# Optimization experiments

Hardware: AMD Instinct MI355X
Metric: run time of the kernel (lower is better)

Reference implementation:

```python
import jax, jax.numpy as jnp
import numpy as np

N, E = 100000, 1600000
DIMS = [128, 64, 64, 64, 32]  # in, hid, hid, hid, out
NEG_SLOPE = 0.2               # GATv2Conv default negative_slope
ELU_ALPHA_OUT = float(DIMS[-1])  # nn.ELU(out_channels): alpha = out_channels


def setup_inputs() -> dict:
    key = jax.random.key(0)
    ks = jax.random.split(key, 16)
    inp = {
        "x": jax.random.normal(ks[0], (N, DIMS[0]), dtype=jnp.float32),
        "edge_index": jax.random.randint(ks[1], (2, E), 0, N, dtype=jnp.int64),
    }
    ki = 2
    for i in range(4):
        fin, fout = DIMS[i], DIMS[i + 1]
        s = 1.0 / np.sqrt(fin)
        inp[f"Wl{i+1}"] = jax.random.uniform(ks[ki], (fin, fout), jnp.float32, -s, s); ki += 1
        inp[f"Wr{i+1}"] = jax.random.uniform(ks[ki], (fin, fout), jnp.float32, -s, s); ki += 1
        inp[f"att{i+1}"] = jax.random.uniform(ks[ki], (fout,), jnp.float32, -s, s); ki += 1
    return inp


def gatv2_layer(x, src, dst, Wl, Wr, att):
    # single head, concat=False, no self-loops, no bias (per module config)
    xl = x @ Wl                                   # [N, F] source-side projection
    xr = x @ Wr                                   # [N, F] target-side projection
    e = jax.nn.leaky_relu(xl[src] + xr[dst], NEG_SLOPE)   # [E, F]
    score = e @ att                               # [E]
    # softmax over incoming edges of each destination node
    m = jax.ops.segment_max(score, dst, num_segments=N)    # [N]
    ex = jnp.exp(score - m[dst])                  # [E]
    denom = jax.ops.segment_sum(ex, dst, num_segments=N)   # [N]
    alpha = ex / (denom[dst] + 1e-16)             # [E]
    # scatter-add weighted source messages
    return jax.ops.segment_sum(xl[src] * alpha[:, None], dst, num_segments=N)


def reference(x, edge_index, Wl1, Wr1, att1, Wl2, Wr2, att2, Wl3, Wr3, att3, Wl4, Wr4, att4):
    src, dst = edge_index[0], edge_index[1]
    h = jax.nn.elu(gatv2_layer(x, src, dst, Wl1, Wr1, att1))
    h = jax.nn.elu(gatv2_layer(h, src, dst, Wl2, Wr2, att2))
    h = jax.nn.elu(gatv2_layer(h, src, dst, Wl3, Wr3, att3))
    h = gatv2_layer(h, src, dst, Wl4, Wr4, att4)
    # nn.ELU(out_channels) -> ELU with alpha = out_channels (faithful quirk)
    return jnp.where(h > 0, h, ELU_ALPHA_OUT * jnp.expm1(h))
```

## Files before the change

### kernel.cpp

```cpp
#include <hip/hip_runtime.h>
#include <math.h>

typedef __attribute__((ext_vector_type(8))) short bf16x8;
typedef __attribute__((ext_vector_type(4))) float f32x4;
typedef __attribute__((ext_vector_type(2))) _Float16 h2;

#define BSHIFT 7
#define CH 8192

__device__ inline unsigned short f32_to_bf16_bits(float f) {
    unsigned int u = __float_as_uint(f);
    unsigned int r = (u + 0x7fffu + ((u >> 16) & 1u)) >> 16;
    return (unsigned short)r;
}
__device__ inline float bf16_bits_to_f32(unsigned short h) {
    return __uint_as_float(((unsigned int)h) << 16);
}
__device__ inline h2 u2h(unsigned u) { return __builtin_bit_cast(h2, u); }
__device__ inline unsigned h2u(h2 h) { return __builtin_bit_cast(unsigned, h); }

#define SWZ_ADD(t, imm) \
    t += __int_as_float(__builtin_amdgcn_ds_swizzle(__float_as_int(t), imm))

__device__ inline float dot2acc(h2 a, h2 b, float c) {
#if defined(__has_builtin)
#if __has_builtin(__builtin_amdgcn_fdot2)
    return __builtin_amdgcn_fdot2(a, b, c, false);
#else
    return c + (float)a[0] * (float)b[0] + (float)a[1] * (float)b[1];
#endif
#else
    return c + (float)a[0] * (float)b[0] + (float)a[1] * (float)b[1];
#endif
}


__global__ __launch_bounds__(256) void bucket_hist(
    const int* __restrict__ dst, int* __restrict__ bh, int E, int nb, int nbp)
{
    __shared__ int h[1024];
    for (int i = threadIdx.x; i < nb; i += 256) h[i] = 0;
    __syncthreads();
    int e0 = blockIdx.x * CH, e1 = min(e0 + CH, E);
    for (int e = e0 + (int)threadIdx.x; e < e1; e += 256)
        atomicAdd(&h[dst[e] >> BSHIFT], 1);
    __syncthreads();
    for (int b = threadIdx.x; b < nb; b += 256)
        bh[(size_t)blockIdx.x * nbp + b] = h[b];
}

__global__ void bucket_scan(int* __restrict__ bh, int* __restrict__ bbase,
                            int* __restrict__ rowstart,
                            int nb, int nbp, int kgrid, int E, int N)
{
    __shared__ int sh[1024];
    int t = threadIdx.x;
    int run = 0;
    if (t < nb) {
        for (int b = 0; b < kgrid; ++b) {
            int* p = &bh[(size_t)b * nbp + t];
            int v = *p;
            *p = run;
            run += v;
        }
    }
    sh[t] = run;
    __syncthreads();
    for (int d = 1; d < 1024; d <<= 1) {
        int a = (t >= d) ? sh[t - d] : 0;
        __syncthreads();
        sh[t] += a;
        __syncthreads();
    }
    int base = sh[t] - run;
    if (t < nb) {
        bbase[t] = base;
        for (int b = 0; b < kgrid; ++b) bh[(size_t)b * nbp + t] += base;
    }
    if (t == nb) bbase[t] = E;
    if (t == 0) rowstart[N] = E;
}

__global__ __launch_bounds__(256) void bucket_scatter(
    const int* __restrict__ src, const int* __restrict__ dst,
    const int* __restrict__ bh, unsigned* __restrict__ pairs, int E, int nb, int nbp)
{
    __shared__ int cur[1024];
    for (int i = threadIdx.x; i < nb; i += 256)
        cur[i] = bh[(size_t)blockIdx.x * nbp + i];
    __syncthreads();
    int e0 = blockIdx.x * CH, e1 = min(e0 + CH, E);
    for (int e = e0 + (int)threadIdx.x; e < e1; e += 256) {
        int d = dst[e];
        int pos = atomicAdd(&cur[d >> BSHIFT], 1);
        pairs[pos] = ((unsigned)src[e] << BSHIFT) | (unsigned)(d & 127);
    }
}

__global__ __launch_bounds__(256) void bucket_finalize(
    const unsigned* __restrict__ pairs, const int* __restrict__ bbase,
    int* __restrict__ rowstart, int* __restrict__ csr_src, int N)
{
    __shared__ int h[128];
    __shared__ int sh[256];
    int b = blockIdx.x;
    int p0 = bbase[b], p1 = bbase[b + 1];
    int t = threadIdx.x;
    if (t < 128) h[t] = 0;
    __syncthreads();
    for (int e = p0 + t; e < p1; e += 256)
        atomicAdd(&h[pairs[e] & 127], 1);
    __syncthreads();
    int v = (t < 128) ? h[t] : 0;
    sh[t] = v;
    __syncthreads();
    for (int d = 1; d < 256; d <<= 1) {
        int a = (t >= d) ? sh[t - d] : 0;
        __syncthreads();
        sh[t] += a;
        __syncthreads();
    }
    if (t < 128) {
        int off = sh[t] - v;
        int node = (b << BSHIFT) + t;
        if (node < N) rowstart[node] = p0 + off;
        h[t] = p0 + off;
    }
    __syncthreads();
    for (int e = p0 + t; e < p1; e += 256) {
        unsigned pr = pairs[e];
        int pos = atomicAdd(&h[pr & 127], 1);
        csr_src[pos] = (int)(pr >> BSHIFT);
    }
}


__device__ inline void prepack_one(const float* __restrict__ W, unsigned short* __restrict__ P,
                                   int FIN, int FOUT, int ii) {
    int NT = FOUT >> 4, NK = FIN >> 5;
    int part = NT * NK * 512;
    int j = ii & 7;
    int lane = (ii >> 3) & 63;
    int rest = ii >> 9;
    int ks = rest % NK;
    int t = rest / NK;
    int k = ks * 32 + (lane >> 4) * 8 + j;
    int c = t * 16 + (lane & 15);
    float w = W[(size_t)k * FOUT + c];
    unsigned short hi = f32_to_bf16_bits(w);
    unsigned short lo = f32_to_bf16_bits(w - bf16_bits_to_f32(hi));
    P[ii] = hi;
    P[part + ii] = lo;
}

__global__ void prepack_all(
    const float* Wl1, const float* Wr1, const float* Wl2, const float* Wr2,
    const float* Wl3, const float* Wr3, const float* Wl4, const float* Wr4,
    unsigned short* pWl1, unsigned short* pWr1, unsigned short* pWl2, unsigned short* pWr2,
    unsigned short* pWl3, unsigned short* pWr3, unsigned short* pWl4, unsigned short* pWr4)
{
    int i = blockIdx.x * 256 + threadIdx.x;
    if      (i < 8192)  prepack_one(Wl1, pWl1, 128, 64, i);
    else if (i < 16384) prepack_one(Wr1, pWr1, 128, 64, i - 8192);
    else if (i < 20480) prepack_one(Wl2, pWl2, 64, 64, i - 16384);
    else if (i < 24576) prepack_one(Wr2, pWr2, 64, 64, i - 20480);
    else if (i < 28672) prepack_one(Wl3, pWl3, 64, 64, i - 24576);
    else if (i < 32768) prepack_one(Wr3, pWr3, 64, 64, i - 28672);
    else if (i < 34816) prepack_one(Wl4, pWl4, 64, 32, i - 32768);
    else if (i < 36864) prepack_one(Wr4, pWr4, 64, 32, i - 34816);
}


template<int FIN, int FOUT, bool IN16>
__global__ __launch_bounds__(256) void proj_mfma_kernel(
    const void* __restrict__ xin,
    const unsigned short* __restrict__ pWl, const unsigned short* __restrict__ pWr,
    const float* __restrict__ att,
    _Float16* __restrict__ xlh, _Float16* __restrict__ xrh,
    float* __restrict__ dl, float* __restrict__ dr, int n)
{
    constexpr int NT = FOUT >> 4;
    constexpr int NK = FIN >> 5;
    constexpr int PART = NT * NK * 512;
    const int wave = threadIdx.x >> 6;
    const int lane = threadIdx.x & 63;
    const int row0 = blockIdx.x * 64 + wave * 16;
    int arow = row0 + (lane & 15);
    if (arow >= n) arow = n - 1;
    const int khalf = lane >> 4;

    f32x4 accl[NT], accr[NT];
#pragma unroll
    for (int t = 0; t < NT; ++t) {
        accl[t] = (f32x4){0.f, 0.f, 0.f, 0.f};
        accr[t] = (f32x4){0.f, 0.f, 0.f, 0.f};
    }

#pragma unroll
    for (int ks = 0; ks < NK; ++ks) {
        float av[8];
        if (IN16) {
            const _Float16* xrow = (const _Float16*)xin + (size_t)arow * FIN + khalf * 8;
            float4 raw = *(const float4*)(xrow + ks * 32);
            const unsigned* u = (const unsigned*)&raw;
#pragma unroll
            for (int j = 0; j < 4; ++j) {
                h2 p = u2h(u[j]);
                av[2 * j]     = (float)p[0];
                av[2 * j + 1] = (float)p[1];
            }
        } else {
            const float* xrow = (const float*)xin + (size_t)arow * FIN + khalf * 8;
            float4 a0 = *(const float4*)(xrow + ks * 32);
            float4 a1 = *(const float4*)(xrow + ks * 32 + 4);
            av[0] = a0.x; av[1] = a0.y; av[2] = a0.z; av[3] = a0.w;
            av[4] = a1.x; av[5] = a1.y; av[6] = a1.z; av[7] = a1.w;
        }
        bf16x8 ah, al;
#pragma unroll
        for (int j = 0; j < 8; ++j) {
            unsigned short h = f32_to_bf16_bits(av[j]);
            ah[j] = (short)h;
            al[j] = (short)f32_to_bf16_bits(av[j] - bf16_bits_to_f32(h));
        }
#pragma unroll
        for (int t = 0; t < NT; ++t) {
            const unsigned short* bpl = pWl + ((size_t)(t * NK + ks) * 64 + lane) * 8;
            bf16x8 bh  = *(const bf16x8*)bpl;
            bf16x8 blo = *(const bf16x8*)(bpl + PART);
            accl[t] = __builtin_amdgcn_mfma_f32_16x16x32_bf16(ah, bh,  accl[t], 0, 0, 0);
            accl[t] = __builtin_amdgcn_mfma_f32_16x16x32_bf16(ah, blo, accl[t], 0, 0, 0);
            accl[t] = __builtin_amdgcn_mfma_f32_16x16x32_bf16(al, bh,  accl[t], 0, 0, 0);
            const unsigned short* bpr = pWr + ((size_t)(t * NK + ks) * 64 + lane) * 8;
            bh  = *(const bf16x8*)bpr;
            blo = *(const bf16x8*)(bpr + PART);
            accr[t] = __builtin_amdgcn_mfma_f32_16x16x32_bf16(ah, bh,  accr[t], 0, 0, 0);
            accr[t] = __builtin_amdgcn_mfma_f32_16x16x32_bf16(ah, blo, accr[t], 0, 0, 0);
            accr[t] = __builtin_amdgcn_mfma_f32_16x16x32_bf16(al, bh,  accr[t], 0, 0, 0);
        }
    }

    const int orow0 = row0 + khalf * 4;
    const int colb = lane & 15;
    float attc[NT];
#pragma unroll
    for (int t = 0; t < NT; ++t) attc[t] = att[t * 16 + colb];

#pragma unroll
    for (int t = 0; t < NT; ++t) {
        int col = t * 16 + colb;
#pragma unroll
        for (int r = 0; r < 4; ++r) {
            int rr = orow0 + r;
            if (rr < n) {
                xlh[(size_t)rr * FOUT + col] = (_Float16)accl[t][r];
                xrh[(size_t)rr * FOUT + col] = (_Float16)accr[t][r];
            }
        }
    }
#pragma unroll
    for (int r = 0; r < 4; ++r) {
        float pl = 0.f, pr = 0.f;
#pragma unroll
        for (int t = 0; t < NT; ++t) { pl += accl[t][r] * attc[t]; pr += accr[t][r] * attc[t]; }
#pragma unroll
        for (int off = 1; off < 16; off <<= 1) {
            pl += __shfl_xor(pl, off);
            pr += __shfl_xor(pr, off);
        }
        int rr = orow0 + r;
        if (colb == 0 && rr < n) { dl[rr] = pl; dr[rr] = pr; }
    }
}


template<int F, int AMODE, bool OUT16>
__global__ __launch_bounds__(256) void agg_kernel(
    const _Float16* __restrict__ xlh, const _Float16* __restrict__ xrh,
    const float* __restrict__ att,
    const float* __restrict__ dl, const float* __restrict__ dr,
    const int* __restrict__ rowstart, const int* __restrict__ csr_src,
    void* __restrict__ outv, int n, int E, int ntiles)
{
    constexpr int LPE = F / 8;
    constexpr int LSH = (F == 64) ? 6 : 5;
    constexpr int NPG = 64 / LPE;

    int wv0  = (blockIdx.x * blockDim.x + threadIdx.x) >> 6;
    int nwaves = gridDim.x * (blockDim.x >> 6);
    int lane = threadIdx.x & 63;
    int grp = lane / LPE;
    int fl  = lane % LPE;

    h2 atth[4];
#pragma unroll
    for (int j = 0; j < 4; ++j) {
        atth[j][0] = (_Float16)att[fl * 8 + 2 * j];
        atth[j][1] = (_Float16)att[fl * 8 + 2 * j + 1];
    }

    for (int tile = wv0; tile < ntiles; tile += nwaves) {
        int node = tile * NPG + grp;
        bool act = node < n;
        int nc = act ? node : 0;

        float4 xrraw = *(const float4*)(xrh + (((unsigned)nc << LSH) + fl * 8));
        h2 xrv[4];
#pragma unroll
        for (int j = 0; j < 4; ++j) xrv[j] = u2h(((const unsigned*)&xrraw)[j]);
        float cdr = 0.6f * dr[nc];

        int s0 = rowstart[nc];
        int s1 = act ? rowstart[nc + 1] : s0;

        float m = -1e30f, mth = -1e30f, ssum = 0.f;
        float o[8];
#pragma unroll
        for (int j = 0; j < 8; ++j) o[j] = 0.f;

        int cA0 = csr_src[s0];
        int cB0 = csr_src[s0 + 1];
        int cA1 = csr_src[s0 + 2];
        int cB1 = csr_src[s0 + 3];
        float4 rA0 = *(const float4*)(xlh + (((unsigned)cA0 << LSH) + fl * 8));
        float4 rB0 = *(const float4*)(xlh + (((unsigned)cB0 << LSH) + fl * 8));
        float  dA0 = dl[cA0], dB0 = dl[cB0];
        float4 rA1 = *(const float4*)(xlh + (((unsigned)cA1 << LSH) + fl * 8));
        float4 rB1 = *(const float4*)(xlh + (((unsigned)cB1 << LSH) + fl * 8));
        float  dA1 = dl[cA1], dB1 = dl[cB1];
        int fA0 = csr_src[s0 + 4];
        int fB0 = csr_src[s0 + 5];
        int fA1 = csr_src[s0 + 6];
        int fB1 = csr_src[s0 + 7];

        int i0 = s0;

#define AGG_COMPUTE(RA, RB, DA, DB)                                          \
        {                                                                    \
            h2 a[4], b[4];                                                   \
            _Pragma("unroll")                                                \
            for (int j = 0; j < 4; ++j) {                                    \
                a[j] = u2h(((const unsigned*)&RA)[j]);                       \
                b[j] = u2h(((const unsigned*)&RB)[j]);                       \
            }                                                                \
            bool vb = (i0 + 1) < s1;                                         \
            float ta = 0.f, tb = 0.f;                                        \
            _Pragma("unroll")                                                \
            for (int j = 0; j < 4; ++j) {                                    \
                h2 ea = a[j] + xrv[j];                                       \
                h2 eb = b[j] + xrv[j];                                       \
                ea = u2h(h2u(ea) & 0x7FFF7FFFu);                             \
                eb = u2h(h2u(eb) & 0x7FFF7FFFu);                             \
                ta = dot2acc(atth[j], ea, ta);                               \
                tb = dot2acc(atth[j], eb, tb);                               \
            }                                                                \
            SWZ_ADD(ta, 0x041F); SWZ_ADD(tb, 0x041F);                        \
            SWZ_ADD(ta, 0x081F); SWZ_ADD(tb, 0x081F);                        \
            if (LPE == 8) { SWZ_ADD(ta, 0x101F); SWZ_ADD(tb, 0x101F); }      \
            float pa = 0.6f * DA + cdr + 0.4f * ta;                          \
            float pb = vb ? (0.6f * DB + cdr + 0.4f * tb) : -1e30f;          \
            float pm = fmaxf(pa, pb);                                        \
            if (pm > mth) {                                                  \
                float c = __expf(m - pm);                                    \
                ssum *= c;                                                   \
                _Pragma("unroll")                                            \
                for (int j = 0; j < 8; ++j) o[j] *= c;                       \
                m = pm; mth = pm + 8.0f;                                     \
            }                                                                \
            float wa = __expf(pa - m);                                       \
            float wb = __expf(pb - m);                                       \
            ssum += wa + wb;                                                 \
            _Pragma("unroll")                                                \
            for (int j = 0; j < 4; ++j) {                                    \
                o[2 * j]     += wa * (float)a[j][0] + wb * (float)b[j][0];   \
                o[2 * j + 1] += wa * (float)a[j][1] + wb * (float)b[j][1];   \
            }                                                                \
        }

        while (i0 < s1) {
            {
                int cA2 = fA0, cB2 = fB0;
                fA0 = csr_src[i0 + 8];
                fB0 = csr_src[i0 + 9];
                AGG_COMPUTE(rA0, rB0, dA0, dB0);
                rA0 = *(const float4*)(xlh + (((unsigned)cA2 << LSH) + fl * 8));
                rB0 = *(const float4*)(xlh + (((unsigned)cB2 << LSH) + fl * 8));
                dA0 = dl[cA2]; dB0 = dl[cB2];
            }
            i0 += 2;
            if (i0 >= s1) break;
            {
                int cA2 = fA1, cB2 = fB1;
                fA1 = csr_src[i0 + 8];
                fB1 = csr_src[i0 + 9];
                AGG_COMPUTE(rA1, rB1, dA1, dB1);
                rA1 = *(const float4*)(xlh + (((unsigned)cA2 << LSH) + fl * 8));
                rB1 = *(const float4*)(xlh + (((unsigned)cB2 << LSH) + fl * 8));
                dA1 = dl[cA2]; dB1 = dl[cB2];
            }
            i0 += 2;
        }
#undef AGG_COMPUTE

        float inv = 1.f / (ssum + 1e-16f);
        float res[8];
#pragma unroll
        for (int j = 0; j < 8; ++j) {
            float r = o[j] * inv;
            if (AMODE == 1) r = (r > 0.f) ? r : expm1f(r);
            else            r = (r > 0.f) ? r : 32.f * expm1f(r);
            res[j] = r;
        }
        if (act) {
            if (OUT16) {
                unsigned pk[4];
#pragma unroll
                for (int j = 0; j < 4; ++j) {
                    h2 t;
                    t[0] = (_Float16)res[2 * j];
                    t[1] = (_Float16)res[2 * j + 1];
                    pk[j] = h2u(t);
                }
                _Float16* op = (_Float16*)outv + (((unsigned)node << LSH) + fl * 8);
                *(float4*)op = *(const float4*)pk;
            } else {
                float* op = (float*)outv + (((unsigned)node << LSH) + fl * 8);
                *(float4*)op       = (float4){res[0], res[1], res[2], res[3]};
                *(float4*)(op + 4) = (float4){res[4], res[5], res[6], res[7]};
            }
        }
    }
}


extern "C" void kernel_launch(void* const* d_in, const int* in_sizes, int n_in,
                              void* d_out, int out_size, void* d_ws, size_t ws_size,
                              hipStream_t stream) {
    const float* x    = (const float*)d_in[0];
    const int*   ei   = (const int*)d_in[1];
    const float* Wl1  = (const float*)d_in[2];
    const float* Wr1  = (const float*)d_in[3];
    const float* att1 = (const float*)d_in[4];
    const float* Wl2  = (const float*)d_in[5];
    const float* Wr2  = (const float*)d_in[6];
    const float* att2 = (const float*)d_in[7];
    const float* Wl3  = (const float*)d_in[8];
    const float* Wr3  = (const float*)d_in[9];
    const float* att3 = (const float*)d_in[10];
    const float* Wl4  = (const float*)d_in[11];
    const float* Wr4  = (const float*)d_in[12];
    const float* att4 = (const float*)d_in[13];

    const int N = in_sizes[0] / 128;
    const int E = in_sizes[1] / 2;
    const int* src = ei;
    const int* dst = ei + E;

    const int nb  = (N + 127) >> BSHIFT;
    const int nbp = (nb + 15) & ~15;
    const int kgrid = (E + CH - 1) / CH;

    char* w = (char*)d_ws;
    size_t off = 0;
    auto take = [&](size_t bytes) -> void* {
        void* p = w + off;
        off = (off + bytes + 255) & ~(size_t)255;
        return p;
    };
    int* bh       = (int*)take((size_t)kgrid * nbp * 4);
    int* bbase    = (int*)take((size_t)(nb + 1) * 4);
    int* rowstart = (int*)take((size_t)(N + 1) * 4);
    int* csr_src  = (int*)take((size_t)(E + 16) * 4);
    float* dl = (float*)take((size_t)N * 4);
    float* dr = (float*)take((size_t)N * 4);
    _Float16* xlh = (_Float16*)take((size_t)N * 64 * 2);
    _Float16* xrh = (_Float16*)take((size_t)N * 64 * 2);
    _Float16* hA  = (_Float16*)take((size_t)N * 64 * 2);
    _Float16* hB  = (_Float16*)take((size_t)N * 64 * 2);
    unsigned short* pWl1 = (unsigned short*)take(2 * 4 * 4 * 512 * 2);
    unsigned short* pWr1 = (unsigned short*)take(2 * 4 * 4 * 512 * 2);
    unsigned short* pWl2 = (unsigned short*)take(2 * 4 * 2 * 512 * 2);
    unsigned short* pWr2 = (unsigned short*)take(2 * 4 * 2 * 512 * 2);
    unsigned short* pWl3 = (unsigned short*)take(2 * 4 * 2 * 512 * 2);
    unsigned short* pWr3 = (unsigned short*)take(2 * 4 * 2 * 512 * 2);
    unsigned short* pWl4 = (unsigned short*)take(2 * 2 * 2 * 512 * 2);
    unsigned short* pWr4 = (unsigned short*)take(2 * 2 * 2 * 512 * 2);
    unsigned* pairs = (unsigned*)hA;
    float* outf = (float*)d_out;

    hipMemsetAsync(csr_src + E, 0, 16 * 4, stream);

    prepack_all<<<144, 256, 0, stream>>>(Wl1, Wr1, Wl2, Wr2, Wl3, Wr3, Wl4, Wr4,
                                         pWl1, pWr1, pWl2, pWr2, pWl3, pWr3, pWl4, pWr4);

    bucket_hist<<<kgrid, 256, 0, stream>>>(dst, bh, E, nb, nbp);
    bucket_scan<<<1, 1024, 0, stream>>>(bh, bbase, rowstart, nb, nbp, kgrid, E, N);
    bucket_scatter<<<kgrid, 256, 0, stream>>>(src, dst, bh, pairs, E, nb, nbp);
    bucket_finalize<<<nb, 256, 0, stream>>>(pairs, bbase, rowstart, csr_src, N);

    int pblk = (N + 63) / 64;
    const int AGGB = 2048;
    int nt64 = (N + 7) / 8;
    int nt32 = (N + 15) / 16;

    proj_mfma_kernel<128, 64, false><<<pblk, 256, 0, stream>>>(x, pWl1, pWr1, att1, xlh, xrh, dl, dr, N);
    agg_kernel<64, 1, true><<<AGGB, 256, 0, stream>>>(xlh, xrh, att1, dl, dr, rowstart, csr_src, hA, N, E, nt64);

    proj_mfma_kernel<64, 64, true><<<pblk, 256, 0, stream>>>(hA, pWl2, pWr2, att2, xlh, xrh, dl, dr, N);
    agg_kernel<64, 1, true><<<AGGB, 256, 0, stream>>>(xlh, xrh, att2, dl, dr, rowstart, csr_src, hB, N, E, nt64);

    proj_mfma_kernel<64, 64, true><<<pblk, 256, 0, stream>>>(hB, pWl3, pWr3, att3, xlh, xrh, dl, dr, N);
    agg_kernel<64, 1, true><<<AGGB, 256, 0, stream>>>(xlh, xrh, att3, dl, dr, rowstart, csr_src, hA, N, E, nt64);

    proj_mfma_kernel<64, 32, true><<<pblk, 256, 0, stream>>>(hA, pWl4, pWr4, att4, xlh, xrh, dl, dr, N);
    agg_kernel<32, 2, false><<<AGGB, 256, 0, stream>>>(xlh, xrh, att4, dl, dr, rowstart, csr_src, outf, N, E, nt32);
}
```

Before: 357.0 us.

## Parallelize bucket histogram scan across waves and fold base offset into scatter

```diff
diff --git a/kernel.cpp b/kernel.cpp
--- a/kernel.cpp
+++ b/kernel.cpp
@@ -49,22 +49,36 @@
         bh[(size_t)blockIdx.x * nbp + b] = h[b];
 }
 
-__global__ void bucket_scan(int* __restrict__ bh, int* __restrict__ bbase,
-                            int* __restrict__ rowstart,
-                            int nb, int nbp, int kgrid, int E, int N)
+__global__ __launch_bounds__(256) void bucket_scanA(
+    int* __restrict__ bh, int* __restrict__ btot, int nb, int nbp, int kgrid)
+{
+    int wv = (blockIdx.x * 256 + threadIdx.x) >> 6;
+    int lane = threadIdx.x & 63;
+    if (wv >= nb) return;
+    int run = 0;
+    for (int b0 = 0; b0 < kgrid; b0 += 64) {
+        int b = b0 + lane;
+        int v = (b < kgrid) ? bh[(size_t)b * nbp + wv] : 0;
+        int s = v;
+#pragma unroll
+        for (int off = 1; off < 64; off <<= 1) {
+            int u = __shfl_up(s, off);
+            if (lane >= off) s += u;
+        }
+        int excl = s - v + run;
+        if (b < kgrid) bh[(size_t)b * nbp + wv] = excl;
+        run += __shfl(s, 63);
+    }
+    if (lane == 0) btot[wv] = run;
+}
+
+__global__ void bucket_scanB(const int* __restrict__ btot, int* __restrict__ bbase,
+                             int* __restrict__ rowstart, int nb, int E, int N)
 {
     __shared__ int sh[1024];
     int t = threadIdx.x;
-    int run = 0;
-    if (t < nb) {
-        for (int b = 0; b < kgrid; ++b) {
-            int* p = &bh[(size_t)b * nbp + t];
-            int v = *p;
-            *p = run;
-            run += v;
-        }
-    }
-    sh[t] = run;
+    int v = (t < nb) ? btot[t] : 0;
+    sh[t] = v;
     __syncthreads();
     for (int d = 1; d < 1024; d <<= 1) {
         int a = (t >= d) ? sh[t - d] : 0;
@@ -72,22 +86,19 @@
         sh[t] += a;
         __syncthreads();
     }
-    int base = sh[t] - run;
-    if (t < nb) {
-        bbase[t] = base;
-        for (int b = 0; b < kgrid; ++b) bh[(size_t)b * nbp + t] += base;
-    }
+    if (t < nb) bbase[t] = sh[t] - v;
     if (t == nb) bbase[t] = E;
     if (t == 0) rowstart[N] = E;
 }
 
 __global__ __launch_bounds__(256) void bucket_scatter(
     const int* __restrict__ src, const int* __restrict__ dst,
-    const int* __restrict__ bh, unsigned* __restrict__ pairs, int E, int nb, int nbp)
+    const int* __restrict__ bh, const int* __restrict__ bbase,
+    unsigned* __restrict__ pairs, int E, int nb, int nbp)
 {
     __shared__ int cur[1024];
     for (int i = threadIdx.x; i < nb; i += 256)
-        cur[i] = bh[(size_t)blockIdx.x * nbp + i];
+        cur[i] = bh[(size_t)blockIdx.x * nbp + i] + bbase[i];
     __syncthreads();
     int e0 = blockIdx.x * CH, e1 = min(e0 + CH, E);
     for (int e = e0 + (int)threadIdx.x; e < e1; e += 256) {
@@ -468,6 +479,7 @@
         return p;
     };
     int* bh       = (int*)take((size_t)kgrid * nbp * 4);
+    int* btot     = (int*)take((size_t)nbp * 4);
     int* bbase    = (int*)take((size_t)(nb + 1) * 4);
     int* rowstart = (int*)take((size_t)(N + 1) * 4);
     int* csr_src  = (int*)take((size_t)(E + 16) * 4);
@@ -494,8 +506,9 @@
                                          pWl1, pWr1, pWl2, pWr2, pWl3, pWr3, pWl4, pWr4);
 
     bucket_hist<<<kgrid, 256, 0, stream>>>(dst, bh, E, nb, nbp);
-    bucket_scan<<<1, 1024, 0, stream>>>(bh, bbase, rowstart, nb, nbp, kgrid, E, N);
-    bucket_scatter<<<kgrid, 256, 0, stream>>>(src, dst, bh, pairs, E, nb, nbp);
+    bucket_scanA<<<(nb + 3) / 4, 256, 0, stream>>>(bh, btot, nb, nbp, kgrid);
+    bucket_scanB<<<1, 1024, 0, stream>>>(btot, bbase, rowstart, nb, E, N);
+    bucket_scatter<<<kgrid, 256, 0, stream>>>(src, dst, bh, bbase, pairs, E, nb, nbp);
     bucket_finalize<<<nb, 256, 0, stream>>>(pairs, bbase, rowstart, csr_src, N);
 
     int pblk = (N + 63) / 64;
```

After: 290.2 us. 1.23x faster.
